# Kernel optimization log

Measured on AMD Instinct MI355X. Metric: run time of the kernel, lower is better.

## Reference

```python
import jax, jax.numpy as jnp
import numpy as np

D_MODEL = 1024
NUM_HEADS = 16
D_K = D_MODEL // NUM_HEADS
NEG_INF = -1000000000.0


def setup_inputs() -> dict:
    key = jax.random.key(0)
    ks = jax.random.split(key, 12)
    B, S = 4, 2048
    scale = 1.0 / np.sqrt(D_MODEL)
    inp = {
        "query": jax.random.normal(ks[0], (B, S, D_MODEL), dtype=jnp.float32),
        "key": jax.random.normal(ks[1], (B, S, D_MODEL), dtype=jnp.float32),
        "value": jax.random.normal(ks[2], (B, S, D_MODEL), dtype=jnp.float32),
        # causal mask: True = keep (matches mask == False -> -1e9 fill)
        "mask": jnp.tril(jnp.ones((S, S), dtype=bool)),
        # torch nn.Linear: y = x @ W.T + b, W shape [out, in]
        "Wq": jax.random.normal(ks[3], (D_MODEL, D_MODEL), dtype=jnp.float32) * scale,
        "bq": jnp.zeros((D_MODEL,), dtype=jnp.float32),
        "Wk": jax.random.normal(ks[4], (D_MODEL, D_MODEL), dtype=jnp.float32) * scale,
        "bk": jnp.zeros((D_MODEL,), dtype=jnp.float32),
        "Wv": jax.random.normal(ks[5], (D_MODEL, D_MODEL), dtype=jnp.float32) * scale,
        "bv": jnp.zeros((D_MODEL,), dtype=jnp.float32),
        "Wo": jax.random.normal(ks[6], (D_MODEL, D_MODEL), dtype=jnp.float32) * scale,
        "bo": jnp.zeros((D_MODEL,), dtype=jnp.float32),
    }
    return inp


def _split_heads(x):
    # [B, S, D] -> [B, H, S, d_k]
    B, S, _ = x.shape
    return x.reshape(B, S, NUM_HEADS, D_K).transpose(0, 2, 1, 3)


def reference(query, key, value, mask, Wq, bq, Wk, bk, Wv, bv, Wo, bo):
    B, S, _ = query.shape
    q = _split_heads(query @ Wq.T + bq)
    k = _split_heads(key @ Wk.T + bk)
    v = _split_heads(value @ Wv.T + bv)
    # scores: [B, H, Sq, Sk]
    scores = jnp.einsum("bhqd,bhkd->bhqk", q, k) / jnp.sqrt(jnp.float32(D_K))
    scores = jnp.where(mask[None, None, :, :], scores, NEG_INF)
    p_attn = jax.nn.softmax(scores, axis=-1)
    x = jnp.einsum("bhqk,bhkd->bhqd", p_attn, v)
    x = x.transpose(0, 2, 1, 3).reshape(B, S, D_MODEL)
    return x @ Wo.T + bo
```

## Files before the change

kernel.cpp:

```cpp
#include <hip/hip_runtime.h>
#include <cstdint>
#include <cstddef>


typedef __attribute__((ext_vector_type(8))) short bf16x8;
typedef __attribute__((ext_vector_type(4))) float f32x4;
typedef __attribute__((ext_vector_type(16))) float f32x16;

__device__ __forceinline__ unsigned short f2bf(float f) {
  union { float f; unsigned u; } x; x.f = f;
  unsigned r = x.u + 0x7FFFu + ((x.u >> 16) & 1u);
  return (unsigned short)(r >> 16);
}

__device__ __forceinline__ unsigned cvtpk_bf16(float lo, float hi) {
  unsigned r;
  asm("v_cvt_pk_bf16_f32 %0, %1, %2" : "=v"(r) : "v"(lo), "v"(hi));
  return r;
}

__device__ __forceinline__ f32x16 mfma32(bf16x8 a, bf16x8 b, f32x16 c) {
  return __builtin_amdgcn_mfma_f32_32x32x16_bf16(a, b, c, 0, 0, 0);
}

__device__ __forceinline__ void gld16(unsigned short* lds, const unsigned short* g) {
  __builtin_amdgcn_global_load_lds(
      (const __attribute__((address_space(1))) unsigned int*)g,
      (__attribute__((address_space(3))) unsigned int*)lds, 16, 0, 0);
}

__global__ __launch_bounds__(256)
void cast_w(const float* __restrict__ wq, const float* __restrict__ wk,
            const float* __restrict__ wv, const float* __restrict__ wo,
            unsigned short* __restrict__ wqb, unsigned short* __restrict__ wkb,
            unsigned short* __restrict__ wvb, unsigned short* __restrict__ wob) {
  constexpr int W4 = 1024 * 1024 / 4;
  const int i = blockIdx.x * 256 + threadIdx.x;
  const int r = i / W4;
  const int off = i - r * W4;
  const float* src = (r == 0) ? wq : (r == 1) ? wk : (r == 2) ? wv : wo;
  unsigned short* dst = (r == 0) ? wqb : (r == 1) ? wkb : (r == 2) ? wvb : wob;
  const float4 f = ((const float4*)src)[off];
  ushort4 o;
  o.x = f2bf(f.x); o.y = f2bf(f.y); o.z = f2bf(f.z); o.w = f2bf(f.w);
  ((ushort4*)dst)[off] = o;
}

template <bool F32OUT, bool SCALEQ, bool CASTA, bool TRANSV>
__global__ __launch_bounds__(256)
void gemm_bt(const void* __restrict__ Ap,
             const unsigned short* __restrict__ Bw,
             const float* __restrict__ bias,
             unsigned short* __restrict__ Cb,
             float* __restrict__ Cf,
             int M, int N, int K) {
  __shared__ unsigned short As[128 * 64];
  __shared__ unsigned short Bs[128 * 64];
  const int tid = threadIdx.x;
  const int lane = tid & 63;
  const int w = tid >> 6;
  const int wm = (w >> 1) * 64;
  const int wn = (w & 1) * 64;
  const int bid = blockIdx.x;
  const int xcd = bid & 7, jj = bid >> 3;
  const int m0 = (xcd * 8 + (jj >> 3)) * 128;
  const int n0 = (jj & 7) * 128;
  const int l15 = lane & 15, l4 = lane >> 4;

  const float* Af = (const float*)Ap;
  const unsigned short* Ab = (const unsigned short*)Ap;

  f32x4 acc[4][4] = {};

  for (int k0 = 0; k0 < K; k0 += 64) {
    if constexpr (CASTA) {
      float4 av[4][2];
#pragma unroll
      for (int q = 0; q < 4; ++q) {
        const int c = q * 256 + tid;
        const int row = c >> 3, kc = (c & 7) * 8;
        const float4* ap = (const float4*)(Af + (size_t)(m0 + row) * K + k0 + kc);
        av[q][0] = ap[0];
        av[q][1] = ap[1];
      }
      __syncthreads();
#pragma unroll
      for (int q = 0; q < 4; ++q) {
        const int c = q * 256 + tid;
        union { bf16x8 v; unsigned u[4]; } p;
        p.u[0] = cvtpk_bf16(av[q][0].x, av[q][0].y);
        p.u[1] = cvtpk_bf16(av[q][0].z, av[q][0].w);
        p.u[2] = cvtpk_bf16(av[q][1].x, av[q][1].y);
        p.u[3] = cvtpk_bf16(av[q][1].z, av[q][1].w);
        *(bf16x8*)&As[c * 8] = p.v;
      }
#pragma unroll
      for (int q = 0; q < 4; ++q) {
        const int c = q * 256 + tid;
        const int row = c >> 3, kc = (c & 7) * 8;
        gld16(&Bs[c * 8], &Bw[(size_t)(n0 + row) * K + k0 + kc]);
      }
      __syncthreads();
    } else {
      __syncthreads();
#pragma unroll
      for (int q = 0; q < 4; ++q) {
        const int c = q * 256 + tid;
        const int row = c >> 3, kc = (c & 7) * 8;
        gld16(&As[c * 8], &Ab[(size_t)(m0 + row) * K + k0 + kc]);
        gld16(&Bs[c * 8], &Bw[(size_t)(n0 + row) * K + k0 + kc]);
      }
      __syncthreads();
    }

#pragma unroll
    for (int kk = 0; kk < 2; ++kk) {
      bf16x8 af[4], bfr[4];
#pragma unroll
      for (int m = 0; m < 4; ++m)
        af[m] = *(const bf16x8*)&As[(wm + m * 16 + l15) * 64 + kk * 32 + l4 * 8];
#pragma unroll
      for (int n = 0; n < 4; ++n)
        bfr[n] = *(const bf16x8*)&Bs[(wn + n * 16 + l15) * 64 + kk * 32 + l4 * 8];
#pragma unroll
      for (int m = 0; m < 4; ++m)
#pragma unroll
        for (int n = 0; n < 4; ++n)
          acc[m][n] = __builtin_amdgcn_mfma_f32_16x16x32_bf16(af[m], bfr[n], acc[m][n], 0, 0, 0);
    }
  }

  const int crow = l4 * 4;
#pragma unroll
  for (int m = 0; m < 4; ++m) {
#pragma unroll
    for (int n = 0; n < 4; ++n) {
      const int col = n0 + wn + n * 16 + l15;
      const float bv_ = bias[col];
      if constexpr (TRANSV) {
        constexpr int SS = 2048;
        const int rowb = m0 + wm + m * 16 + crow;
        const int b_ = rowb >> 11, s_ = rowb & (SS - 1);
        const int vrow = ((b_ << 4) + (col >> 6)) * 64 + (col & 63);
        uint2 pk;
        pk.x = cvtpk_bf16(acc[m][n][0] + bv_, acc[m][n][1] + bv_);
        pk.y = cvtpk_bf16(acc[m][n][2] + bv_, acc[m][n][3] + bv_);
        *(uint2*)&Cb[(size_t)vrow * SS + s_] = pk;
      } else {
#pragma unroll
        for (int j = 0; j < 4; ++j) {
          const int row = m0 + wm + m * 16 + crow + j;
          float v = acc[m][n][j] + bv_;
          if constexpr (SCALEQ) v *= 0.125f * 1.44269504f;
          if constexpr (F32OUT) Cf[(size_t)row * N + col] = v;
          else                  Cb[(size_t)row * N + col] = f2bf(v);
        }
      }
    }
  }
}

__global__ __launch_bounds__(256)
void attn_fwd32b(const unsigned short* __restrict__ Qp,
                 const unsigned short* __restrict__ Kp,
                 const unsigned short* __restrict__ Vt,
                 unsigned short* __restrict__ Xo) {
  constexpr int S = 2048, Dm = 1024;
  const int bh = blockIdx.x & 63;
  const int g  = 15 - (int)(blockIdx.x >> 6);
  const int b = bh >> 4, h = bh & 15;
  const int w = threadIdx.x >> 6;
  const int lane = threadIdx.x & 63;
  const int l31 = lane & 31, hi = lane >> 5;
  const int qb = 4 * g + w;
  const int qrow = qb * 32 + l31;
  const int ntw = qb + 1;
  const int NT = 4 * g + 4;

  const unsigned short* qptr = Qp + (size_t)(b * S + qrow) * Dm + h * 64 + hi * 8;
  bf16x8 qf[4];
#pragma unroll
  for (int c = 0; c < 4; ++c) qf[c] = *(const bf16x8*)(qptr + c * 16);

  const unsigned short* kbase = Kp + (size_t)(b * S) * Dm + h * 64 + hi * 8;
  const unsigned short* vr0 = Vt + (size_t)(bh * 64 + l31) * S + hi * 8;
  const unsigned short* vr1 = vr0 + (size_t)32 * S;

  f32x16 ot0 = {}, ot1 = {};
  float m = -1e30f, l = 0.f;

  auto loadK = [&](bf16x8 (&kr)[4], int t) {
    const unsigned short* krow = kbase + (size_t)(t * 32 + l31) * Dm;
#pragma unroll
    for (int c = 0; c < 4; ++c) kr[c] = *(const bf16x8*)(krow + c * 16);
  };

  auto body = [&](bf16x8 (&kr)[4], int t) {
    const int kv0 = t * 32;
    const bf16x8 vf0a = *(const bf16x8*)(vr0 + kv0);
    const bf16x8 vf0b = *(const bf16x8*)(vr0 + kv0 + 16);
    const bf16x8 vf1a = *(const bf16x8*)(vr1 + kv0);
    const bf16x8 vf1b = *(const bf16x8*)(vr1 + kv0 + 16);
    f32x16 ts = {};
#pragma unroll
    for (int c = 0; c < 4; ++c) ts = mfma32(kr[c], qf[c], ts);
    if (t == ntw - 1) {
#pragma unroll
      for (int r = 0; r < 16; ++r) {
        const int kvp = kv0 + (r & 3) + 8 * (r >> 2) + 4 * hi;
        if (kvp > qrow) ts[r] = -1e9f;
      }
    }
    float pmax = ts[0];
#pragma unroll
    for (int r = 1; r < 16; ++r) pmax = fmaxf(pmax, ts[r]);
    pmax = fmaxf(pmax, __shfl_xor(pmax, 32));
    if (__any(pmax > m + 11.5f)) {
      const float mn = (pmax > m + 11.5f) ? pmax : m;
      const float fct = __builtin_amdgcn_exp2f(m - mn);
      m = mn; l *= fct;
#pragma unroll
      for (int r = 0; r < 16; ++r) { ot0[r] *= fct; ot1[r] *= fct; }
    }
    float p[16], ls = 0.f;
#pragma unroll
    for (int r = 0; r < 16; ++r) {
      p[r] = __builtin_amdgcn_exp2f(ts[r] - m);
      ls += p[r];
    }
    ls += __shfl_xor(ls, 32);
    l += ls;
    unsigned ua[8];
#pragma unroll
    for (int i = 0; i < 8; ++i) ua[i] = cvtpk_bf16(p[2 * i], p[2 * i + 1]);
    union FR { bf16x8 v; unsigned u[4]; } fr0, fr1;
    {
      unsigned sa = hi ? ua[0] : ua[2], sb = hi ? ua[1] : ua[3];
      unsigned xa = __shfl_xor(sa, 32), xb = __shfl_xor(sb, 32);
      fr0.u[0] = hi ? xa : ua[0]; fr0.u[1] = hi ? xb : ua[1];
      fr0.u[2] = hi ? ua[2] : xa; fr0.u[3] = hi ? ua[3] : xb;
      unsigned sc = hi ? ua[4] : ua[6], sd = hi ? ua[5] : ua[7];
      unsigned xc = __shfl_xor(sc, 32), xd = __shfl_xor(sd, 32);
      fr1.u[0] = hi ? xc : ua[4]; fr1.u[1] = hi ? xd : ua[5];
      fr1.u[2] = hi ? ua[6] : xc; fr1.u[3] = hi ? ua[7] : xd;
    }
    ot0 = mfma32(vf0a, fr0.v, ot0);
    ot0 = mfma32(vf0b, fr1.v, ot0);
    ot1 = mfma32(vf1a, fr0.v, ot1);
    ot1 = mfma32(vf1b, fr1.v, ot1);
  };

  bf16x8 kA[4], kB[4];
  loadK(kA, 0);
  for (int t = 0; t < NT; t += 2) {
    loadK(kB, t + 1);
    if (t < ntw) body(kA, t);
    __builtin_amdgcn_s_barrier();
    const int t2 = (t + 2 < NT) ? (t + 2) : (NT - 1);
    loadK(kA, t2);
    if (t + 1 < ntw) body(kB, t + 1);
    __builtin_amdgcn_s_barrier();
  }

  const float inv = 1.f / l;
  unsigned short* orow = Xo + (size_t)(b * S + qrow) * Dm + h * 64;
#pragma unroll
  for (int rq = 0; rq < 4; ++rq) {
    uint2 pr;
    pr.x = cvtpk_bf16(ot0[4 * rq + 0] * inv, ot0[4 * rq + 1] * inv);
    pr.y = cvtpk_bf16(ot0[4 * rq + 2] * inv, ot0[4 * rq + 3] * inv);
    *(uint2*)(orow + 8 * rq + 4 * hi) = pr;
    uint2 pr1;
    pr1.x = cvtpk_bf16(ot1[4 * rq + 0] * inv, ot1[4 * rq + 1] * inv);
    pr1.y = cvtpk_bf16(ot1[4 * rq + 2] * inv, ot1[4 * rq + 3] * inv);
    *(uint2*)(orow + 32 + 8 * rq + 4 * hi) = pr1;
  }
}

extern "C" void kernel_launch(void* const* d_in, const int* in_sizes, int n_in,
                              void* d_out, int out_size, void* d_ws, size_t ws_size,
                              hipStream_t stream) {
  const float* query = (const float*)d_in[0];
  const float* key   = (const float*)d_in[1];
  const float* value = (const float*)d_in[2];
  const float* Wq = (const float*)d_in[4];
  const float* bq = (const float*)d_in[5];
  const float* Wk = (const float*)d_in[6];
  const float* bk = (const float*)d_in[7];
  const float* Wv = (const float*)d_in[8];
  const float* bv = (const float*)d_in[9];
  const float* Wo = (const float*)d_in[10];
  const float* bo = (const float*)d_in[11];

  constexpr int B = 4, S = 2048, D = 1024;
  constexpr int M = B * S;
  const size_t MB = 1024u * 1024u;
  uint8_t* ws = (uint8_t*)d_ws;

  unsigned short* Wqb = (unsigned short*)(ws + 48 * MB);
  unsigned short* Wkb = (unsigned short*)(ws + 50 * MB);
  unsigned short* Wvb = (unsigned short*)(ws + 52 * MB);
  unsigned short* Wob = (unsigned short*)(ws + 54 * MB);
  unsigned short* Qp  = (unsigned short*)(ws + 56 * MB);
  unsigned short* Kp  = (unsigned short*)(ws + 72 * MB);
  unsigned short* Vt  = (unsigned short*)(ws + 32 * MB);
  unsigned short* Xat = (unsigned short*)(ws + 16 * MB);

  constexpr int W4 = D * D / 4;
  cast_w<<<4 * W4 / 256, 256, 0, stream>>>(Wq, Wk, Wv, Wo, Wqb, Wkb, Wvb, Wob);

  gemm_bt<false, true , true , false><<<512, 256, 0, stream>>>(query, Wqb, bq, Qp, nullptr, M, D, D);
  gemm_bt<false, false, true , false><<<512, 256, 0, stream>>>(key,   Wkb, bk, Kp, nullptr, M, D, D);
  gemm_bt<false, false, true , true ><<<512, 256, 0, stream>>>(value, Wvb, bv, Vt, nullptr, M, D, D);

  attn_fwd32b<<<1024, 256, 0, stream>>>(Qp, Kp, Vt, Xat);

  gemm_bt<true, false, false, false><<<512, 256, 0, stream>>>(Xat, Wob, bo, nullptr, (float*)d_out, M, D, D);
}
```

Before: 256.6 us.

## Merge Q/K/V projection GEMMs into one launch and raise MFMA wave priority

The three separate QKV projection GEMM launches become a single 1536-block kernel that picks its input, weight, bias and output layout from the block index. This removes two launches and the tail of each 512-block grid, so blocks from all three projections can fill the GPU together. The attention kernel also wraps its MFMA groups in s_setprio(1)/s_setprio(0) so matrix work gets issue priority over other waves. The output GEMM is split into its own specialized kernel. Runtime branching on `which` in the epilogue adds some divergence-free overhead and register pressure.

```diff
diff --git a/kernel.cpp b/kernel.cpp
--- a/kernel.cpp
+++ b/kernel.cpp
@@ -46,14 +46,117 @@
   ((ushort4*)dst)[off] = o;
 }
 
-template <bool F32OUT, bool SCALEQ, bool CASTA, bool TRANSV>
 __global__ __launch_bounds__(256)
-void gemm_bt(const void* __restrict__ Ap,
-             const unsigned short* __restrict__ Bw,
-             const float* __restrict__ bias,
-             unsigned short* __restrict__ Cb,
-             float* __restrict__ Cf,
-             int M, int N, int K) {
+void gemm_qkv(const float* __restrict__ Aq, const float* __restrict__ Ak,
+              const float* __restrict__ Av,
+              const unsigned short* __restrict__ Wq, const unsigned short* __restrict__ Wk,
+              const unsigned short* __restrict__ Wv,
+              const float* __restrict__ bq, const float* __restrict__ bk,
+              const float* __restrict__ bv,
+              unsigned short* __restrict__ Qp, unsigned short* __restrict__ Kp,
+              unsigned short* __restrict__ Vt,
+              int M, int N, int K) {
+  __shared__ unsigned short As[128 * 64];
+  __shared__ unsigned short Bs[128 * 64];
+  const int which = blockIdx.x >> 9;
+  const int bid = blockIdx.x & 511;
+  const float* Af = (which == 0) ? Aq : (which == 1) ? Ak : Av;
+  const unsigned short* Bw = (which == 0) ? Wq : (which == 1) ? Wk : Wv;
+  const float* bias = (which == 0) ? bq : (which == 1) ? bk : bv;
+
+  const int tid = threadIdx.x;
+  const int lane = tid & 63;
+  const int w = tid >> 6;
+  const int wm = (w >> 1) * 64;
+  const int wn = (w & 1) * 64;
+  const int xcd = bid & 7, jj = bid >> 3;
+  const int m0 = (xcd * 8 + (jj >> 3)) * 128;
+  const int n0 = (jj & 7) * 128;
+  const int l15 = lane & 15, l4 = lane >> 4;
+
+  f32x4 acc[4][4] = {};
+
+  for (int k0 = 0; k0 < K; k0 += 64) {
+    float4 av[4][2];
+#pragma unroll
+    for (int q = 0; q < 4; ++q) {
+      const int c = q * 256 + tid;
+      const int row = c >> 3, kc = (c & 7) * 8;
+      const float4* ap = (const float4*)(Af + (size_t)(m0 + row) * K + k0 + kc);
+      av[q][0] = ap[0];
+      av[q][1] = ap[1];
+    }
+    __syncthreads();
+#pragma unroll
+    for (int q = 0; q < 4; ++q) {
+      const int c = q * 256 + tid;
+      union { bf16x8 v; unsigned u[4]; } p;
+      p.u[0] = cvtpk_bf16(av[q][0].x, av[q][0].y);
+      p.u[1] = cvtpk_bf16(av[q][0].z, av[q][0].w);
+      p.u[2] = cvtpk_bf16(av[q][1].x, av[q][1].y);
+      p.u[3] = cvtpk_bf16(av[q][1].z, av[q][1].w);
+      *(bf16x8*)&As[c * 8] = p.v;
+    }
+#pragma unroll
+    for (int q = 0; q < 4; ++q) {
+      const int c = q * 256 + tid;
+      const int row = c >> 3, kc = (c & 7) * 8;
+      gld16(&Bs[c * 8], &Bw[(size_t)(n0 + row) * K + k0 + kc]);
+    }
+    __syncthreads();
+
+#pragma unroll
+    for (int kk = 0; kk < 2; ++kk) {
+      bf16x8 af[4], bfr[4];
+#pragma unroll
+      for (int m = 0; m < 4; ++m)
+        af[m] = *(const bf16x8*)&As[(wm + m * 16 + l15) * 64 + kk * 32 + l4 * 8];
+#pragma unroll
+      for (int n = 0; n < 4; ++n)
+        bfr[n] = *(const bf16x8*)&Bs[(wn + n * 16 + l15) * 64 + kk * 32 + l4 * 8];
+#pragma unroll
+      for (int m = 0; m < 4; ++m)
+#pragma unroll
+        for (int n = 0; n < 4; ++n)
+          acc[m][n] = __builtin_amdgcn_mfma_f32_16x16x32_bf16(af[m], bfr[n], acc[m][n], 0, 0, 0);
+    }
+  }
+
+  const int crow = l4 * 4;
+#pragma unroll
+  for (int m = 0; m < 4; ++m) {
+#pragma unroll
+    for (int n = 0; n < 4; ++n) {
+      const int col = n0 + wn + n * 16 + l15;
+      const float bv_ = bias[col];
+      if (which == 2) {
+        constexpr int SS = 2048;
+        const int rowb = m0 + wm + m * 16 + crow;
+        const int b_ = rowb >> 11, s_ = rowb & (SS - 1);
+        const int vrow = ((b_ << 4) + (col >> 6)) * 64 + (col & 63);
+        uint2 pk;
+        pk.x = cvtpk_bf16(acc[m][n][0] + bv_, acc[m][n][1] + bv_);
+        pk.y = cvtpk_bf16(acc[m][n][2] + bv_, acc[m][n][3] + bv_);
+        *(uint2*)&Vt[(size_t)vrow * SS + s_] = pk;
+      } else {
+        unsigned short* Cb = (which == 0) ? Qp : Kp;
+        const float sc = (which == 0) ? 0.125f * 1.44269504f : 1.0f;
+#pragma unroll
+        for (int j = 0; j < 4; ++j) {
+          const int row = m0 + wm + m * 16 + crow + j;
+          Cb[(size_t)row * N + col] = f2bf((acc[m][n][j] + bv_) * sc);
+        }
+      }
+    }
+  }
+}
+
+__global__ __launch_bounds__(256)
+void gemm_out(const unsigned short* __restrict__ Ab,
+              const unsigned short* __restrict__ Bw,
+              const float* __restrict__ bias,
+              float* __restrict__ Cf,
+              int M, int N, int K) {
   __shared__ unsigned short As[128 * 64];
   __shared__ unsigned short Bs[128 * 64];
   const int tid = threadIdx.x;
@@ -67,51 +170,18 @@
   const int n0 = (jj & 7) * 128;
   const int l15 = lane & 15, l4 = lane >> 4;
 
-  const float* Af = (const float*)Ap;
-  const unsigned short* Ab = (const unsigned short*)Ap;
-
   f32x4 acc[4][4] = {};
 
   for (int k0 = 0; k0 < K; k0 += 64) {
-    if constexpr (CASTA) {
-      float4 av[4][2];
-#pragma unroll
-      for (int q = 0; q < 4; ++q) {
-        const int c = q * 256 + tid;
-        const int row = c >> 3, kc = (c & 7) * 8;
-        const float4* ap = (const float4*)(Af + (size_t)(m0 + row) * K + k0 + kc);
-        av[q][0] = ap[0];
-        av[q][1] = ap[1];
-      }
-      __syncthreads();
-#pragma unroll
-      for (int q = 0; q < 4; ++q) {
-        const int c = q * 256 + tid;
-        union { bf16x8 v; unsigned u[4]; } p;
-        p.u[0] = cvtpk_bf16(av[q][0].x, av[q][0].y);
-        p.u[1] = cvtpk_bf16(av[q][0].z, av[q][0].w);
-        p.u[2] = cvtpk_bf16(av[q][1].x, av[q][1].y);
-        p.u[3] = cvtpk_bf16(av[q][1].z, av[q][1].w);
-        *(bf16x8*)&As[c * 8] = p.v;
-      }
-#pragma unroll
-      for (int q = 0; q < 4; ++q) {
-        const int c = q * 256 + tid;
-        const int row = c >> 3, kc = (c & 7) * 8;
-        gld16(&Bs[c * 8], &Bw[(size_t)(n0 + row) * K + k0 + kc]);
-      }
-      __syncthreads();
-    } else {
-      __syncthreads();
-#pragma unroll
-      for (int q = 0; q < 4; ++q) {
-        const int c = q * 256 + tid;
-        const int row = c >> 3, kc = (c & 7) * 8;
-        gld16(&As[c * 8], &Ab[(size_t)(m0 + row) * K + k0 + kc]);
-        gld16(&Bs[c * 8], &Bw[(size_t)(n0 + row) * K + k0 + kc]);
-      }
-      __syncthreads();
-    }
+    __syncthreads();
+#pragma unroll
+    for (int q = 0; q < 4; ++q) {
+      const int c = q * 256 + tid;
+      const int row = c >> 3, kc = (c & 7) * 8;
+      gld16(&As[c * 8], &Ab[(size_t)(m0 + row) * K + k0 + kc]);
+      gld16(&Bs[c * 8], &Bw[(size_t)(n0 + row) * K + k0 + kc]);
+    }
+    __syncthreads();
 
 #pragma unroll
     for (int kk = 0; kk < 2; ++kk) {
@@ -137,24 +207,10 @@
     for (int n = 0; n < 4; ++n) {
       const int col = n0 + wn + n * 16 + l15;
       const float bv_ = bias[col];
-      if constexpr (TRANSV) {
-        constexpr int SS = 2048;
-        const int rowb = m0 + wm + m * 16 + crow;
-        const int b_ = rowb >> 11, s_ = rowb & (SS - 1);
-        const int vrow = ((b_ << 4) + (col >> 6)) * 64 + (col & 63);
-        uint2 pk;
-        pk.x = cvtpk_bf16(acc[m][n][0] + bv_, acc[m][n][1] + bv_);
-        pk.y = cvtpk_bf16(acc[m][n][2] + bv_, acc[m][n][3] + bv_);
-        *(uint2*)&Cb[(size_t)vrow * SS + s_] = pk;
-      } else {
-#pragma unroll
-        for (int j = 0; j < 4; ++j) {
-          const int row = m0 + wm + m * 16 + crow + j;
-          float v = acc[m][n][j] + bv_;
-          if constexpr (SCALEQ) v *= 0.125f * 1.44269504f;
-          if constexpr (F32OUT) Cf[(size_t)row * N + col] = v;
-          else                  Cb[(size_t)row * N + col] = f2bf(v);
-        }
+#pragma unroll
+      for (int j = 0; j < 4; ++j) {
+        const int row = m0 + wm + m * 16 + crow + j;
+        Cf[(size_t)row * N + col] = acc[m][n][j] + bv_;
       }
     }
   }
@@ -202,8 +258,10 @@
     const bf16x8 vf1a = *(const bf16x8*)(vr1 + kv0);
     const bf16x8 vf1b = *(const bf16x8*)(vr1 + kv0 + 16);
     f32x16 ts = {};
+    __builtin_amdgcn_s_setprio(1);
 #pragma unroll
     for (int c = 0; c < 4; ++c) ts = mfma32(kr[c], qf[c], ts);
+    __builtin_amdgcn_s_setprio(0);
     if (t == ntw - 1) {
 #pragma unroll
       for (int r = 0; r < 16; ++r) {
@@ -244,10 +302,12 @@
       fr1.u[0] = hi ? xc : ua[4]; fr1.u[1] = hi ? xd : ua[5];
       fr1.u[2] = hi ? ua[6] : xc; fr1.u[3] = hi ? ua[7] : xd;
     }
+    __builtin_amdgcn_s_setprio(1);
     ot0 = mfma32(vf0a, fr0.v, ot0);
     ot0 = mfma32(vf0b, fr1.v, ot0);
     ot1 = mfma32(vf1a, fr0.v, ot1);
     ot1 = mfma32(vf1b, fr1.v, ot1);
+    __builtin_amdgcn_s_setprio(0);
   };
 
   bf16x8 kA[4], kB[4];
@@ -309,11 +369,10 @@
   constexpr int W4 = D * D / 4;
   cast_w<<<4 * W4 / 256, 256, 0, stream>>>(Wq, Wk, Wv, Wo, Wqb, Wkb, Wvb, Wob);
 
-  gemm_bt<false, true , true , false><<<512, 256, 0, stream>>>(query, Wqb, bq, Qp, nullptr, M, D, D);
-  gemm_bt<false, false, true , false><<<512, 256, 0, stream>>>(key,   Wkb, bk, Kp, nullptr, M, D, D);
-  gemm_bt<false, false, true , true ><<<512, 256, 0, stream>>>(value, Wvb, bv, Vt, nullptr, M, D, D);
+  gemm_qkv<<<1536, 256, 0, stream>>>(query, key, value, Wqb, Wkb, Wvb,
+                                     bq, bk, bv, Qp, Kp, Vt, M, D, D);
 
   attn_fwd32b<<<1024, 256, 0, stream>>>(Qp, Kp, Vt, Xat);
 
-  gemm_bt<true, false, false, false><<<512, 256, 0, stream>>>(Xat, Wob, bo, nullptr, (float*)d_out, M, D, D);
-}
+  gemm_out<<<512, 256, 0, stream>>>(Xat, Wob, bo, (float*)d_out, M, D, D);
+}
```

Measured after the change: 253.6 us. No clear change (-1.2%).
